# Kernel tuning notes

Measured on AMD Instinct MI355X. Metric: run time of the kernel, lower is better.

Reference implementation:

```python
import jax, jax.numpy as jnp
import numpy as np

CHUNK = 128  # intra-chunk causal block size for the chunked linear-attention scan


def setup_inputs() -> dict:
    key = jax.random.key(0)
    ks = jax.random.split(key, 7)
    B, H, N, D, F = 1, 24, 4096, 128, 256
    q = jax.random.normal(ks[0], (B, H, N, D), dtype=jnp.float32)
    k = jax.random.normal(ks[1], (B, H, N, D), dtype=jnp.float32)
    v = jax.random.normal(ks[2], (B, H, N, D), dtype=jnp.float32)
    # fan-in scaling so phi features / accumulated state stay numerically sane
    w1 = jax.random.normal(ks[3], (F, D), dtype=jnp.float32) * (D ** -0.5)
    b1 = jax.random.normal(ks[4], (F,), dtype=jnp.float32) * 0.02
    w2 = jax.random.normal(ks[5], (F, F), dtype=jnp.float32) * (F ** -0.5)
    b2 = jax.random.normal(ks[6], (F,), dtype=jnp.float32) * 0.02
    return {"q": q, "k": k, "v": v, "w1": w1, "b1": b1, "w2": w2, "b2": b2}


def _phi(x, w1, b1, w2, b2):
    # Linear(D->F) -> SiLU -> Linear(F->F)
    h = jax.nn.silu(jnp.einsum('bnd,fd->bnf', x, w1) + b1)
    return jnp.einsum('bnf,gf->bng', h, w2) + b2


def _causal_scan(qp, kp, vf):
    # out_t = q_t . (sum_{s<=t} k_s v_s^T) / (t+1), chunked parallel form.
    BH, N, F = qp.shape
    D = vf.shape[-1]
    C = CHUNK
    nC = N // C
    qc = qp.reshape(BH, nC, C, F).transpose(1, 0, 2, 3)  # [nC,BH,C,F]
    kc = kp.reshape(BH, nC, C, F).transpose(1, 0, 2, 3)
    vc = vf.reshape(BH, nC, C, D).transpose(1, 0, 2, 3)
    offsets = (jnp.arange(nC) * C).astype(qp.dtype)
    mask = jnp.tril(jnp.ones((C, C), dtype=qp.dtype))  # include diagonal
    pos = jnp.arange(1, C + 1, dtype=qp.dtype)

    def step(w, inp):
        qb, kb, vb, off = inp
        inter = jnp.einsum('bcf,bfd->bcd', qb, w)
        attn = jnp.einsum('bcf,bsf->bcs', qb, kb) * mask
        intra = jnp.einsum('bcs,bsd->bcd', attn, vb)
        counts = off + pos  # global (token_idx + 1)
        out = (inter + intra) / counts[None, :, None]
        w = w + jnp.einsum('bcf,bcd->bfd', kb, vb)
        return w, out

    w0 = jnp.zeros((BH, F, D), dtype=qp.dtype)
    _, outs = jax.lax.scan(step, w0, (qc, kc, vc, offsets))  # outs [nC,BH,C,D]
    return outs.transpose(1, 0, 2, 3).reshape(BH, N, D)


def reference(q, k, v, w1, b1, w2, b2):
    B, H, N, D = q.shape
    qf = q.reshape(B * H, N, D)
    kf = k.reshape(B * H, N, D)
    vf = v.reshape(B * H, N, D)
    qp = _phi(qf, w1, b1, w2, b2)
    kp = _phi(kf, w1, b1, w2, b2)
    out_fwd = _causal_scan(qp, kp, vf)
    out_rev = _causal_scan(qp[:, ::-1], kp[:, ::-1], vf[:, ::-1])[:, ::-1]
    return (out_fwd + out_rev).reshape(B, H, N, D)
```

## Files before the change

kernel.cpp:

```cpp
#include <hip/hip_runtime.h>


typedef __attribute__((ext_vector_type(8))) _Float16 f16x8;
typedef __attribute__((ext_vector_type(4))) _Float16 f16x4;
typedef __attribute__((ext_vector_type(4))) float f32x4;

#define MFMA16(a, b, c) __builtin_amdgcn_mfma_f32_16x16x32_f16((a), (b), (c), 0, 0, 0)

constexpr int BH   = 24;
constexpr int NSEQ = 4096;
constexpr int DD   = 128;
constexpr int FF   = 256;
constexpr int CHK  = 128;
constexpr int NC   = NSEQ / CHK;
constexpr int NROWS = BH * NSEQ;

__global__ void prep_kernel(const float* __restrict__ w1, const float* __restrict__ w2,
                            _Float16* __restrict__ w1h, _Float16* __restrict__ w2h) {
  int i = blockIdx.x * 256 + threadIdx.x;
  if (i < FF * DD) w1h[i] = (_Float16)w1[i];
  if (i < FF * FF) w2h[i] = (_Float16)w2[i];
}

__global__ void vt_kernel(const float* __restrict__ v, _Float16* __restrict__ vT) {
  __shared__ __align__(16) _Float16 lt[128][136];
  int blk = blockIdx.x;
  int c = blk & 31, bh = blk >> 5;
  const float* vc = v + ((size_t)bh * NSEQ + c * CHK) * DD;
  int tid = threadIdx.x;
#pragma unroll
  for (int it = 0; it < 16; ++it) {
    int flat = it * 1024 + tid * 4;
    int s = flat >> 7, d0 = flat & 127;
    float4 xv = *(const float4*)&vc[(size_t)s * DD + d0];
    lt[d0 + 0][s] = (_Float16)xv.x;
    lt[d0 + 1][s] = (_Float16)xv.y;
    lt[d0 + 2][s] = (_Float16)xv.z;
    lt[d0 + 3][s] = (_Float16)xv.w;
  }
  __syncthreads();
#pragma unroll
  for (int it = 0; it < 8; ++it) {
    int flat = it * 256 + tid;
    int d = flat >> 4, sg = flat & 15;
    *(f16x8*)&vT[((size_t)bh * DD + d) * NSEQ + c * CHK + sg * 8] =
        *(const f16x8*)&lt[d][sg * 8];
  }
}

__global__ __launch_bounds__(512, 8)
void phi_kernel(const float* __restrict__ q, const float* __restrict__ k,
                const float* __restrict__ b1, const float* __restrict__ b2,
                const _Float16* __restrict__ w1h, const _Float16* __restrict__ w2h,
                _Float16* __restrict__ qp, _Float16* __restrict__ kp,
                _Float16* __restrict__ kpT) {
  __shared__ __align__(16) char smem[34816];
  _Float16 (*xs)[136] = (_Float16(*)[136])smem;
  _Float16 (*hs)[264] = (_Float16(*)[264])smem;
  _Float16 (*os)[264] = (_Float16(*)[264])smem;
  _Float16 (*ot)[68]  = (_Float16(*)[68])smem;
  int blk = blockIdx.x;
  const float* src;
  _Float16* dst;
  bool isk = (blk & 1);
  int rb = (blk >> 1) * 64;
  if (!isk) { src = q; dst = qp; }
  else      { src = k; dst = kp; }
  int tid = threadIdx.x;
  int lane = tid & 63, wv = tid >> 6, lr = lane & 15, lq = lane >> 4;
  int wm = wv & 1, wn = wv >> 1;

#pragma unroll
  for (int it = 0; it < 4; ++it) {
    int flat = it * 512 + tid;
    int r = flat >> 5, dg = flat & 31;
    float4 xv = *(const float4*)&src[(size_t)(rb + r) * DD + dg * 4];
    f16x4 hv = {(_Float16)xv.x, (_Float16)xv.y, (_Float16)xv.z, (_Float16)xv.w};
    *(f16x4*)&xs[r][dg * 4] = hv;
  }
  __syncthreads();

  f32x4 acc[2][4] = {};
#pragma unroll
  for (int ks = 0; ks < 4; ++ks) {
    f16x8 bv[4];
#pragma unroll
    for (int fn = 0; fn < 4; ++fn)
      bv[fn] = *(const f16x8*)&w1h[(size_t)(wn * 64 + fn * 16 + lr) * DD + ks * 32 + lq * 8];
    f16x8 av[2];
#pragma unroll
    for (int im = 0; im < 2; ++im)
      av[im] = *(const f16x8*)&xs[wm * 32 + im * 16 + lr][ks * 32 + lq * 8];
#pragma unroll
    for (int fn = 0; fn < 4; ++fn)
#pragma unroll
      for (int im = 0; im < 2; ++im) acc[im][fn] = MFMA16(av[im], bv[fn], acc[im][fn]);
  }
  __syncthreads();

#pragma unroll
  for (int im = 0; im < 2; ++im)
#pragma unroll
    for (int fn = 0; fn < 4; ++fn) {
      int f = wn * 64 + fn * 16 + lr;
      float bb = b1[f];
      int r0 = wm * 32 + im * 16 + lq * 4;
#pragma unroll
      for (int r = 0; r < 4; ++r) {
        float xv = acc[im][fn][r] + bb;
        hs[r0 + r][f] = (_Float16)(xv * __builtin_amdgcn_rcpf(1.0f + __expf(-xv)));
      }
    }
  __syncthreads();

  f32x4 ac2[2][4] = {};
#pragma unroll
  for (int ks = 0; ks < 8; ++ks) {
    f16x8 bv[4];
#pragma unroll
    for (int fn = 0; fn < 4; ++fn)
      bv[fn] = *(const f16x8*)&w2h[(size_t)(wn * 64 + fn * 16 + lr) * FF + ks * 32 + lq * 8];
    f16x8 av[2];
#pragma unroll
    for (int im = 0; im < 2; ++im)
      av[im] = *(const f16x8*)&hs[wm * 32 + im * 16 + lr][ks * 32 + lq * 8];
#pragma unroll
    for (int fn = 0; fn < 4; ++fn)
#pragma unroll
      for (int im = 0; im < 2; ++im) ac2[im][fn] = MFMA16(av[im], bv[fn], ac2[im][fn]);
  }
  __syncthreads();

  int bh = rb >> 12, s0 = rb & 4095;
#pragma unroll
  for (int im = 0; im < 2; ++im)
#pragma unroll
    for (int fn = 0; fn < 4; ++fn) {
      int g = wn * 64 + fn * 16 + lr;
      float bb = b2[g];
      int r0 = wm * 32 + im * 16 + lq * 4;
#pragma unroll
      for (int r = 0; r < 4; ++r)
        os[r0 + r][g] = (_Float16)(ac2[im][fn][r] + bb);
    }
  __syncthreads();
#pragma unroll
  for (int it = 0; it < 4; ++it) {
    int flat = it * 512 + tid;
    int r = flat >> 5, cg = flat & 31;
    *(f16x8*)&dst[(size_t)(rb + r) * FF + cg * 8] = *(const f16x8*)&os[r][cg * 8];
  }

  if (isk) {
    __syncthreads();
#pragma unroll
    for (int im = 0; im < 2; ++im)
#pragma unroll
      for (int fn = 0; fn < 4; ++fn) {
        int g = wn * 64 + fn * 16 + lr;
        float bb = b2[g];
        int r0 = wm * 32 + im * 16 + lq * 4;
#pragma unroll
        for (int r = 0; r < 4; ++r)
          ot[g][r0 + r] = (_Float16)(ac2[im][fn][r] + bb);
      }
    __syncthreads();
#pragma unroll
    for (int it = 0; it < 4; ++it) {
      int flat = it * 512 + tid;
      int f = flat >> 3, sg = flat & 7;
      *(f16x8*)&kpT[((size_t)bh * FF + f) * NSEQ + s0 + sg * 8] = *(const f16x8*)&ot[f][sg * 8];
    }
  }
}

__global__ __launch_bounds__(512, 2)
void s_kernel(const _Float16* __restrict__ vT, const _Float16* __restrict__ kpT,
              _Float16* __restrict__ S) {
  __shared__ __align__(16) _Float16 vt[128][136];
  __shared__ __align__(16) _Float16 kt[256][136];
  int blk = blockIdx.x;
  int c = blk & 31, bh = blk >> 5;
  int tid = threadIdx.x;
#pragma unroll
  for (int it = 0; it < 4; ++it) {
    int flat = it * 512 + tid;
    int d = flat >> 4, sg = flat & 15;
    *(f16x8*)&vt[d][sg * 8] = *(const f16x8*)&vT[((size_t)bh * DD + d) * NSEQ + c * CHK + sg * 8];
  }
#pragma unroll
  for (int it = 0; it < 8; ++it) {
    int flat = it * 512 + tid;
    int f = flat >> 4, sg = flat & 15;
    *(f16x8*)&kt[f][sg * 8] = *(const f16x8*)&kpT[((size_t)bh * FF + f) * NSEQ + c * CHK + sg * 8];
  }
  __syncthreads();
  int lane = tid & 63, wv = tid >> 6, lr = lane & 15, lq = lane >> 4;
  int wmd = wv & 1, wnf = wv >> 1;
  f32x4 acc[4][4] = {};
#pragma unroll
  for (int ks = 0; ks < 4; ++ks) {
    f16x8 av[4];
#pragma unroll
    for (int im = 0; im < 4; ++im)
      av[im] = *(const f16x8*)&vt[wmd * 64 + im * 16 + lr][ks * 32 + lq * 8];
#pragma unroll
    for (int fn = 0; fn < 4; ++fn) {
      f16x8 bv = *(const f16x8*)&kt[wnf * 64 + fn * 16 + lr][ks * 32 + lq * 8];
#pragma unroll
      for (int im = 0; im < 4; ++im) acc[im][fn] = MFMA16(av[im], bv, acc[im][fn]);
    }
  }
  _Float16* Sp = S + ((size_t)bh * NC + c) * (size_t)(DD * FF);
#pragma unroll
  for (int im = 0; im < 4; ++im)
#pragma unroll
    for (int fn = 0; fn < 4; ++fn) {
      int f = wnf * 64 + fn * 16 + lr;
#pragma unroll
      for (int r = 0; r < 4; ++r) {
        int d = wmd * 64 + im * 16 + lq * 4 + r;
        Sp[(size_t)d * FF + f] = (_Float16)acc[im][fn][r];
      }
    }
}

__global__ void prefix_kernel(_Float16* S_Wr, _Float16* __restrict__ Wf) {
  size_t idx = (size_t)blockIdx.x * 256 + threadIdx.x;
  int bh = (int)(idx >> 15);
  int df = (int)(idx & 32767);
  size_t base = (size_t)bh * NC * 32768 + df;
  float vals[NC];
#pragma unroll
  for (int c = 0; c < NC; ++c) vals[c] = (float)S_Wr[base + (size_t)c * 32768];
  float run = 0.f;
#pragma unroll
  for (int c = 0; c < NC; ++c) { Wf[base + (size_t)c * 32768] = (_Float16)run; run += vals[c]; }
  run = 0.f;
#pragma unroll
  for (int c = NC - 1; c >= 0; --c) { S_Wr[base + (size_t)c * 32768] = (_Float16)run; run += vals[c]; }
}

__global__ __launch_bounds__(512, 2)
void scan_kernel(const _Float16* __restrict__ qp, const _Float16* __restrict__ kp,
                 const _Float16* __restrict__ vT, const _Float16* __restrict__ Wf,
                 const _Float16* __restrict__ Wr, float* __restrict__ out) {
  __shared__ __align__(16) _Float16 vt[128][136];
  __shared__ __align__(16) _Float16 P[128][136];
  int blk = blockIdx.x;
  int c = blk & 31, bh = blk >> 5;
  const _Float16* qpc = qp + ((size_t)bh * NSEQ + c * CHK) * FF;
  const _Float16* kpc = kp + ((size_t)bh * NSEQ + c * CHK) * FF;
  int tid = threadIdx.x, lane = tid & 63, wv = tid >> 6, lr = lane & 15, lq = lane >> 4;
  int wm = wv & 3, wn = wv >> 2;

  f16x8 aq[2][8];
#pragma unroll
  for (int im = 0; im < 2; ++im)
#pragma unroll
    for (int ks = 0; ks < 8; ++ks)
      aq[im][ks] = *(const f16x8*)&qpc[(size_t)(wm * 32 + im * 16 + lr) * FF + ks * 32 + lq * 8];
#pragma unroll
  for (int it = 0; it < 4; ++it) {
    int flat = it * 512 + tid;
    int d = flat >> 4, sg = flat & 15;
    *(f16x8*)&vt[d][sg * 8] = *(const f16x8*)&vT[((size_t)bh * DD + d) * NSEQ + c * CHK + sg * 8];
  }
  f16x8 bk[2][8];
#pragma unroll
  for (int ks = 0; ks < 8; ++ks)
    bk[0][ks] = *(const f16x8*)&kpc[(size_t)(wn * 64 + lr) * FF + ks * 32 + lq * 8];
  f32x4 pacc[2][4] = {};
#pragma unroll
  for (int j = 0; j < 4; ++j) {
    int cur = j & 1;
    if (j < 3)
#pragma unroll
      for (int ks = 0; ks < 8; ++ks)
        bk[cur ^ 1][ks] = *(const f16x8*)&kpc[(size_t)(wn * 64 + (j + 1) * 16 + lr) * FF + ks * 32 + lq * 8];
#pragma unroll
    for (int ks = 0; ks < 8; ++ks)
#pragma unroll
      for (int im = 0; im < 2; ++im)
        pacc[im][j] = MFMA16(aq[im][ks], bk[cur][ks], pacc[im][j]);
  }
#pragma unroll
  for (int im = 0; im < 2; ++im)
#pragma unroll
    for (int j = 0; j < 4; ++j)
#pragma unroll
      for (int r = 0; r < 4; ++r)
        P[wm * 32 + im * 16 + lq * 4 + r][wn * 64 + j * 16 + lr] = (_Float16)pacc[im][j][r];

  const _Float16* Wfc = Wf + ((size_t)bh * NC + c) * (size_t)(DD * FF);
  const _Float16* Wrc = Wr + ((size_t)bh * NC + c) * (size_t)(DD * FF);
  f16x8 bf[8], br[8];
#pragma unroll
  for (int ks = 0; ks < 8; ++ks) {
    int d = wn * 64 + lr;
    bf[ks] = *(const f16x8*)&Wfc[(size_t)d * FF + ks * 32 + lq * 8];
    br[ks] = *(const f16x8*)&Wrc[(size_t)d * FF + ks * 32 + lq * 8];
  }
  __syncthreads();

  f32x4 af[2][4] = {}, ar[2][4] = {};
#pragma unroll
  for (int jd = 0; jd < 4; ++jd) {
#pragma unroll
    for (int ks = 0; ks < 8; ++ks)
#pragma unroll
      for (int im = 0; im < 2; ++im) {
        af[im][jd] = MFMA16(aq[im][ks], bf[ks], af[im][jd]);
        ar[im][jd] = MFMA16(aq[im][ks], br[ks], ar[im][jd]);
      }
    if (jd < 3)
#pragma unroll
      for (int ks = 0; ks < 8; ++ks) {
        int d = wn * 64 + (jd + 1) * 16 + lr;
        bf[ks] = *(const f16x8*)&Wfc[(size_t)d * FF + ks * 32 + lq * 8];
        br[ks] = *(const f16x8*)&Wrc[(size_t)d * FF + ks * 32 + lq * 8];
      }
    {
      int ks = jd;
      f16x8 bv[4];
#pragma unroll
      for (int jd2 = 0; jd2 < 4; ++jd2)
        bv[jd2] = *(const f16x8*)&vt[wn * 64 + jd2 * 16 + lr][ks * 32 + lq * 8];
#pragma unroll
      for (int im = 0; im < 2; ++im) {
        int irow = wm * 32 + im * 16 + lr;
        f16x8 p = *(const f16x8*)&P[irow][ks * 32 + lq * 8];
        f16x8 pf = p, pr = p;
#pragma unroll
        for (int jj = 0; jj < 8; ++jj) {
          int s = ks * 32 + lq * 8 + jj;
          pf[jj] = (s <= irow) ? p[jj] : (_Float16)0.0f;
          pr[jj] = (s >= irow) ? p[jj] : (_Float16)0.0f;
        }
#pragma unroll
        for (int jd2 = 0; jd2 < 4; ++jd2) {
          af[im][jd2] = MFMA16(pf, bv[jd2], af[im][jd2]);
          ar[im][jd2] = MFMA16(pr, bv[jd2], ar[im][jd2]);
        }
      }
    }
  }

  float* oc = out + ((size_t)bh * NSEQ + c * CHK) * DD;
#pragma unroll
  for (int im = 0; im < 2; ++im)
#pragma unroll
    for (int jd = 0; jd < 4; ++jd) {
      int d = wn * 64 + jd * 16 + lr;
#pragma unroll
      for (int r = 0; r < 4; ++r) {
        int il = wm * 32 + im * 16 + lq * 4 + r;
        int gi = c * CHK + il;
        oc[(size_t)il * DD + d] = af[im][jd][r] / (float)(gi + 1) + ar[im][jd][r] / (float)(NSEQ - gi);
      }
    }
}

extern "C" void kernel_launch(void* const* d_in, const int* in_sizes, int n_in,
                              void* d_out, int out_size, void* d_ws, size_t ws_size,
                              hipStream_t stream) {
  const float* q  = (const float*)d_in[0];
  const float* k  = (const float*)d_in[1];
  const float* v  = (const float*)d_in[2];
  const float* w1 = (const float*)d_in[3];
  const float* b1 = (const float*)d_in[4];
  const float* w2 = (const float*)d_in[5];
  const float* b2 = (const float*)d_in[6];
  float* out = (float*)d_out;

  char* ws = (char*)d_ws;
  const size_t SZ = 50331648ull;
  _Float16* w1h = (_Float16*)(ws);
  _Float16* w2h = (_Float16*)(ws + 65536);
  _Float16* qp  = (_Float16*)(ws + 196608);
  _Float16* kp  = (_Float16*)(ws + 196608 + SZ);
  _Float16* kpT = (_Float16*)(ws + 196608 + 2 * SZ);
  _Float16* S   = (_Float16*)(ws + 196608 + 3 * SZ);
  _Float16* vT  = (_Float16*)(ws + 196608 + 4 * SZ);
  _Float16* Wf  = kpT;
  _Float16* Wr  = S;

  prep_kernel<<<dim3(256), dim3(256), 0, stream>>>(w1, w2, w1h, w2h);
  vt_kernel<<<dim3(BH * NC), dim3(256), 0, stream>>>(v, vT);
  phi_kernel<<<dim3(2 * NROWS / 64), dim3(512), 0, stream>>>(q, k, b1, b2, w1h, w2h, qp, kp, kpT);
  s_kernel<<<dim3(BH * NC), dim3(512), 0, stream>>>(vT, kpT, S);
  prefix_kernel<<<dim3(BH * DD * FF / 256), dim3(256), 0, stream>>>(S, Wf);
  scan_kernel<<<dim3(BH * NC), dim3(512), 0, stream>>>(qp, kp, vT, Wf, Wr, out);
}
```

Baseline: 478.1 us.

## Drop kpT buffer; transpose kp in LDS with XOR swizzle inside s_kernel

phi_kernel stops writing a transposed copy of the k features. s_kernel now reads kp row-major and transposes it while storing into shared memory, using an XOR swizzle to reduce bank conflicts on the scattered scalar stores and the later vector reads. phi_kernel also moves to 32-row tiles with 256 threads and preloads biases into registers, raising block count and lowering LDS per block. This removes a full global write of the kp transpose, at the cost of scalar LDS scatter stores in s_kernel.

```diff
diff --git a/kernel.cpp b/kernel.cpp
--- a/kernel.cpp
+++ b/kernel.cpp
@@ -48,31 +48,34 @@
   }
 }
 
-__global__ __launch_bounds__(512, 8)
+__global__ __launch_bounds__(256, 4)
 void phi_kernel(const float* __restrict__ q, const float* __restrict__ k,
                 const float* __restrict__ b1, const float* __restrict__ b2,
                 const _Float16* __restrict__ w1h, const _Float16* __restrict__ w2h,
-                _Float16* __restrict__ qp, _Float16* __restrict__ kp,
-                _Float16* __restrict__ kpT) {
-  __shared__ __align__(16) char smem[34816];
+                _Float16* __restrict__ qp, _Float16* __restrict__ kp) {
+  __shared__ __align__(16) char smem[16896];
   _Float16 (*xs)[136] = (_Float16(*)[136])smem;
   _Float16 (*hs)[264] = (_Float16(*)[264])smem;
   _Float16 (*os)[264] = (_Float16(*)[264])smem;
-  _Float16 (*ot)[68]  = (_Float16(*)[68])smem;
   int blk = blockIdx.x;
-  const float* src;
-  _Float16* dst;
-  bool isk = (blk & 1);
-  int rb = (blk >> 1) * 64;
-  if (!isk) { src = q; dst = qp; }
-  else      { src = k; dst = kp; }
+  bool isk = blk & 1;
+  int rb = (blk >> 1) * 32;
+  const float* src = isk ? k : q;
+  _Float16* dst = isk ? kp : qp;
   int tid = threadIdx.x;
   int lane = tid & 63, wv = tid >> 6, lr = lane & 15, lq = lane >> 4;
-  int wm = wv & 1, wn = wv >> 1;
+  int wn = wv;
+
+  float bb1[4], bb2[4];
+#pragma unroll
+  for (int fn = 0; fn < 4; ++fn) {
+    bb1[fn] = b1[wn * 64 + fn * 16 + lr];
+    bb2[fn] = b2[wn * 64 + fn * 16 + lr];
+  }
 
 #pragma unroll
   for (int it = 0; it < 4; ++it) {
-    int flat = it * 512 + tid;
+    int flat = it * 256 + tid;
     int r = flat >> 5, dg = flat & 31;
     float4 xv = *(const float4*)&src[(size_t)(rb + r) * DD + dg * 4];
     f16x4 hv = {(_Float16)xv.x, (_Float16)xv.y, (_Float16)xv.z, (_Float16)xv.w};
@@ -90,7 +93,7 @@
     f16x8 av[2];
 #pragma unroll
     for (int im = 0; im < 2; ++im)
-      av[im] = *(const f16x8*)&xs[wm * 32 + im * 16 + lr][ks * 32 + lq * 8];
+      av[im] = *(const f16x8*)&xs[im * 16 + lr][ks * 32 + lq * 8];
 #pragma unroll
     for (int fn = 0; fn < 4; ++fn)
 #pragma unroll
@@ -103,11 +106,10 @@
 #pragma unroll
     for (int fn = 0; fn < 4; ++fn) {
       int f = wn * 64 + fn * 16 + lr;
-      float bb = b1[f];
-      int r0 = wm * 32 + im * 16 + lq * 4;
+      int r0 = im * 16 + lq * 4;
 #pragma unroll
       for (int r = 0; r < 4; ++r) {
-        float xv = acc[im][fn][r] + bb;
+        float xv = acc[im][fn][r] + bb1[fn];
         hs[r0 + r][f] = (_Float16)(xv * __builtin_amdgcn_rcpf(1.0f + __expf(-xv)));
       }
     }
@@ -123,7 +125,7 @@
     f16x8 av[2];
 #pragma unroll
     for (int im = 0; im < 2; ++im)
-      av[im] = *(const f16x8*)&hs[wm * 32 + im * 16 + lr][ks * 32 + lq * 8];
+      av[im] = *(const f16x8*)&hs[im * 16 + lr][ks * 32 + lq * 8];
 #pragma unroll
     for (int fn = 0; fn < 4; ++fn)
 #pragma unroll
@@ -131,51 +133,27 @@
   }
   __syncthreads();
 
-  int bh = rb >> 12, s0 = rb & 4095;
 #pragma unroll
   for (int im = 0; im < 2; ++im)
 #pragma unroll
     for (int fn = 0; fn < 4; ++fn) {
       int g = wn * 64 + fn * 16 + lr;
-      float bb = b2[g];
-      int r0 = wm * 32 + im * 16 + lq * 4;
+      int r0 = im * 16 + lq * 4;
 #pragma unroll
       for (int r = 0; r < 4; ++r)
-        os[r0 + r][g] = (_Float16)(ac2[im][fn][r] + bb);
+        os[r0 + r][g] = (_Float16)(ac2[im][fn][r] + bb2[fn]);
     }
   __syncthreads();
 #pragma unroll
   for (int it = 0; it < 4; ++it) {
-    int flat = it * 512 + tid;
+    int flat = it * 256 + tid;
     int r = flat >> 5, cg = flat & 31;
     *(f16x8*)&dst[(size_t)(rb + r) * FF + cg * 8] = *(const f16x8*)&os[r][cg * 8];
   }
-
-  if (isk) {
-    __syncthreads();
-#pragma unroll
-    for (int im = 0; im < 2; ++im)
-#pragma unroll
-      for (int fn = 0; fn < 4; ++fn) {
-        int g = wn * 64 + fn * 16 + lr;
-        float bb = b2[g];
-        int r0 = wm * 32 + im * 16 + lq * 4;
-#pragma unroll
-        for (int r = 0; r < 4; ++r)
-          ot[g][r0 + r] = (_Float16)(ac2[im][fn][r] + bb);
-      }
-    __syncthreads();
-#pragma unroll
-    for (int it = 0; it < 4; ++it) {
-      int flat = it * 512 + tid;
-      int f = flat >> 3, sg = flat & 7;
-      *(f16x8*)&kpT[((size_t)bh * FF + f) * NSEQ + s0 + sg * 8] = *(const f16x8*)&ot[f][sg * 8];
-    }
-  }
 }
 
 __global__ __launch_bounds__(512, 2)
-void s_kernel(const _Float16* __restrict__ vT, const _Float16* __restrict__ kpT,
+void s_kernel(const _Float16* __restrict__ vT, const _Float16* __restrict__ kp,
               _Float16* __restrict__ S) {
   __shared__ __align__(16) _Float16 vt[128][136];
   __shared__ __align__(16) _Float16 kt[256][136];
@@ -191,8 +169,12 @@
 #pragma unroll
   for (int it = 0; it < 8; ++it) {
     int flat = it * 512 + tid;
-    int f = flat >> 4, sg = flat & 15;
-    *(f16x8*)&kt[f][sg * 8] = *(const f16x8*)&kpT[((size_t)bh * FF + f) * NSEQ + c * CHK + sg * 8];
+    int s = flat >> 5, fg = flat & 31;
+    f16x8 kv = *(const f16x8*)&kp[((size_t)bh * NSEQ + c * CHK + s) * FF + fg * 8];
+    int sw = (fg & 15) << 3;
+#pragma unroll
+    for (int j = 0; j < 8; ++j)
+      kt[fg * 8 + j][s ^ sw] = kv[j];
   }
   __syncthreads();
   int lane = tid & 63, wv = tid >> 6, lr = lane & 15, lq = lane >> 4;
@@ -206,7 +188,8 @@
       av[im] = *(const f16x8*)&vt[wmd * 64 + im * 16 + lr][ks * 32 + lq * 8];
 #pragma unroll
     for (int fn = 0; fn < 4; ++fn) {
-      f16x8 bv = *(const f16x8*)&kt[wnf * 64 + fn * 16 + lr][ks * 32 + lq * 8];
+      int F = wnf * 64 + fn * 16 + lr;
+      f16x8 bv = *(const f16x8*)&kt[F][(ks * 32 + lq * 8) ^ (((F >> 3) & 15) << 3)];
 #pragma unroll
       for (int im = 0; im < 4; ++im) acc[im][fn] = MFMA16(av[im], bv, acc[im][fn]);
     }
@@ -379,16 +362,15 @@
   _Float16* w2h = (_Float16*)(ws + 65536);
   _Float16* qp  = (_Float16*)(ws + 196608);
   _Float16* kp  = (_Float16*)(ws + 196608 + SZ);
-  _Float16* kpT = (_Float16*)(ws + 196608 + 2 * SZ);
+  _Float16* Wf  = (_Float16*)(ws + 196608 + 2 * SZ);
   _Float16* S   = (_Float16*)(ws + 196608 + 3 * SZ);
   _Float16* vT  = (_Float16*)(ws + 196608 + 4 * SZ);
-  _Float16* Wf  = kpT;
   _Float16* Wr  = S;
 
   prep_kernel<<<dim3(256), dim3(256), 0, stream>>>(w1, w2, w1h, w2h);
   vt_kernel<<<dim3(BH * NC), dim3(256), 0, stream>>>(v, vT);
-  phi_kernel<<<dim3(2 * NROWS / 64), dim3(512), 0, stream>>>(q, k, b1, b2, w1h, w2h, qp, kp, kpT);
-  s_kernel<<<dim3(BH * NC), dim3(512), 0, stream>>>(vT, kpT, S);
+  phi_kernel<<<dim3(2 * NROWS / 32), dim3(256), 0, stream>>>(q, k, b1, b2, w1h, w2h, qp, kp);
+  s_kernel<<<dim3(BH * NC), dim3(512), 0, stream>>>(vT, kp, S);
   prefix_kernel<<<dim3(BH * DD * FF / 256), dim3(256), 0, stream>>>(S, Wf);
   scan_kernel<<<dim3(BH * NC), dim3(512), 0, stream>>>(qp, kp, vT, Wf, Wr, out);
 }
```

After: 445.2 us. 6.9% less time.
